# Kernel tuning notes

Hardware: AMD Instinct MI355X
Metric: run time of the kernel (lower is better)

## Reference

```python
import jax, jax.numpy as jnp
import numpy as np

NEG_SLOPE = 0.1   # LeakyReLU slope
EPS = 1e-5        # GroupNorm eps
GROUPS = 8        # out_feat // 16 = 128 // 16
NSAMPLE = 16      # naggre (k in KNN)
FEAT = 128        # feat_dim


def leaky(x):
    return jnp.where(x >= 0, x, NEG_SLOPE * x)


def gnorm(x, gamma, beta):
    # GroupNorm over channel dim 1; works for [B,C,N] and [B,C,N,K]
    B, C = x.shape[0], x.shape[1]
    sh = x.shape
    xg = x.reshape(B, GROUPS, -1)
    m = xg.mean(-1, keepdims=True)
    v = xg.var(-1, keepdims=True)
    xg = (xg - m) * jax.lax.rsqrt(v + EPS)
    br = (1, C) + (1,) * (len(sh) - 2)
    return xg.reshape(sh) * gamma.reshape(br) + beta.reshape(br)


def conv1(x, W, b):  # 1x1 Conv1d: x [B,C,N]
    return jnp.einsum('oc,bcn->bon', W, x) + b[None, :, None]


def conv2(x, W, b):  # 1x1 Conv2d: x [B,C,N,K]
    return jnp.einsum('oc,bcnk->bonk', W, x) + b[None, :, None, None]


def knn_idx(xyz, k):
    # xyz [B,3,N] -> idx [B,N,k] of k nearest points (self included)
    pts = xyz.transpose(0, 2, 1)                      # [B,N,3]
    sq = jnp.sum(pts * pts, axis=-1)                  # [B,N]
    d2 = sq[:, :, None] + sq[:, None, :] - 2.0 * jnp.einsum('bnc,bmc->bnm', pts, pts)
    _, idx = jax.lax.top_k(-d2, k)
    return idx


# grouping_operation: feat [B,C,N], idx [B,N,K] -> [B,C,N,K]
group = jax.vmap(lambda f, i: f[:, i])


def setup_inputs() -> dict:
    key = jax.random.key(0)
    ks = jax.random.split(key, 32)
    s = 0.05
    d = {
        'xyz': jax.random.normal(ks[0], (2, 3, 8192), jnp.float32),
        'feat': jax.random.normal(ks[1], (2, FEAT, 8192), jnp.float32),
        'W_pre': jax.random.normal(ks[2], (FEAT, FEAT), jnp.float32) * s,
        'b_pre': jnp.zeros((FEAT,), jnp.float32),
        'W_pos1': jax.random.normal(ks[3], (FEAT, 3), jnp.float32) * s,
        'b_pos1': jnp.zeros((FEAT,), jnp.float32),
        'g_pos1': jnp.ones((FEAT,), jnp.float32),
        'be_pos1': jnp.zeros((FEAT,), jnp.float32),
        'W_pos2': jax.random.normal(ks[4], (FEAT, FEAT), jnp.float32) * s,
        'b_pos2': jnp.zeros((FEAT,), jnp.float32),
        'W_q': jax.random.normal(ks[5], (FEAT, FEAT), jnp.float32) * s,
        'b_q': jnp.zeros((FEAT,), jnp.float32),
        'W_k': jax.random.normal(ks[6], (FEAT, FEAT), jnp.float32) * s,
        'b_k': jnp.zeros((FEAT,), jnp.float32),
        'W_v': jax.random.normal(ks[7], (FEAT, FEAT), jnp.float32) * s,
        'b_v': jnp.zeros((FEAT,), jnp.float32),
        'W_att1': jax.random.normal(ks[8], (FEAT, FEAT), jnp.float32) * s,
        'b_att1': jnp.zeros((FEAT,), jnp.float32),
        'g_att1': jnp.ones((FEAT,), jnp.float32),
        'be_att1': jnp.zeros((FEAT,), jnp.float32),
        'W_att2': jax.random.normal(ks[9], (FEAT, FEAT), jnp.float32) * s,
        'b_att2': jnp.zeros((FEAT,), jnp.float32),
        'W_post': jax.random.normal(ks[10], (FEAT, FEAT), jnp.float32) * s,
        'b_post': jnp.zeros((FEAT,), jnp.float32),
        'g_post': jnp.ones((FEAT,), jnp.float32),
        'be_post': jnp.zeros((FEAT,), jnp.float32),
    }
    return d


def reference(xyz, feat, W_pre, b_pre, W_pos1, b_pos1, g_pos1, be_pos1,
              W_pos2, b_pos2, W_q, b_q, W_k, b_k, W_v, b_v,
              W_att1, b_att1, g_att1, be_att1, W_att2, b_att2,
              W_post, b_post, g_post, be_post):
    idx = knn_idx(xyz, NSAMPLE)                       # [B,N,K]
    new_feat = conv1(feat, W_pre, b_pre)              # [B,C,N]
    rel = group(xyz, idx) - xyz[:, :, :, None]        # [B,3,N,K]
    pos = conv2(rel, W_pos1, b_pos1)
    pos = leaky(gnorm(pos, g_pos1, be_pos1))
    pos = conv2(pos, W_pos2, b_pos2)                  # [B,C,N,K]
    q = conv1(new_feat, W_q, b_q)
    k = group(conv1(new_feat, W_k, b_k), idx)
    v = group(conv1(new_feat, W_v, b_v), idx)
    att = q[:, :, :, None] - k + pos
    att = conv2(att, W_att1, b_att1)
    att = leaky(gnorm(att, g_att1, be_att1))
    att = conv2(att, W_att2, b_att2)
    att = jax.nn.softmax(att, axis=3)                 # softmax over neighbors
    out = jnp.sum(att * v, axis=3) + new_feat         # [B,C,N]
    out = leaky(gnorm(conv1(out, W_post, b_post), g_post, be_post))
    return out
```

## Files before the change

kernel.cpp:

```cpp
#include <hip/hip_runtime.h>
#include <hip/hip_bf16.h>
#include <float.h>

#define B_ 2
#define N_ 8192
#define C_ 128
#define K_ 16
#define G_ 8
#define NK_ (N_*K_)
#define BN_ (B_*N_)
#define BNK_ (B_*NK_)
#define CN_ (C_*N_)
#define NEG 0.1f
#define EPSV 1e-5f

typedef __attribute__((ext_vector_type(4))) float f32x4;
typedef __attribute__((ext_vector_type(8))) short s16x8;
typedef __attribute__((ext_vector_type(4))) short s16x4;

__device__ __forceinline__ float leakyf(float x){ return x >= 0.f ? x : NEG*x; }
__device__ __forceinline__ short f2b(float x){
  union { __hip_bfloat16 b; short s; } u; u.b = __float2bfloat16(x); return u.s;
}
__device__ __forceinline__ float b2f(short s){
  union { __hip_bfloat16 b; short s; } u; u.s = s; return __bfloat162float(u.b);
}

__device__ __forceinline__ int dpp_shr1_i(int x){
  return __builtin_amdgcn_update_dpp(x, x, 0x111, 0xF, 0xF, false);
}
__device__ __forceinline__ unsigned long long dpp_shr1_u64(unsigned long long x){
  union { unsigned long long q; int i[2]; } u; u.q = x;
  u.i[0] = dpp_shr1_i(u.i[0]);
  u.i[1] = dpp_shr1_i(u.i[1]);
  return u.q;
}
__device__ __forceinline__ unsigned long long readlane_u64(unsigned long long x, int l){
  union { unsigned long long q; int i[2]; } u; u.q = x;
  union { unsigned long long q; int i[2]; } r;
  r.i[0] = __builtin_amdgcn_readlane(u.i[0], l);
  r.i[1] = __builtin_amdgcn_readlane(u.i[1], l);
  return r.q;
}
__device__ __forceinline__ unsigned long long d2key(double d2, int idx){
  d2 = fmax(d2, 0.0);
  union { double d; unsigned long long q; } u; u.d = d2;
  return (u.q & ~0x1FFFull) | (unsigned long long)idx;
}
__device__ __forceinline__ double key_upper_d2(unsigned long long k){
  union { unsigned long long q; double d; } u; u.q = k | 0x1FFFull;
  return u.d;
}

__global__ __launch_bounds__(256) void pack_featb_kernel(const float* __restrict__ xyz,
    const float* __restrict__ feat, float4* __restrict__ pt4, ushort* __restrict__ fb){
  int e = blockIdx.x*256 + threadIdx.x;
  int b = e >> 13, n = e & (N_-1);
  const float* xb = xyz + b*3*N_;
  float x = xb[n], y = xb[N_+n], z = xb[2*N_+n];
  pt4[e] = make_float4(x, y, z, x*x + y*y + z*z);
  const float* xin = feat + b*CN_ + n;
  #pragma unroll
  for (int c0 = 0; c0 < C_; c0 += 8){
    s16x8 o8;
    #pragma unroll
    for (int i = 0; i < 8; i++) o8[i] = f2b(xin[(size_t)(c0+i)*N_]);
    *(s16x8*)(fb + (size_t)e*C_ + c0) = o8;
  }
}

#define KNN_TPB 512
#define KNN_CHUNK 2048
#define KNN_MARGIN 2e-4f
__global__ __launch_bounds__(KNN_TPB) void knn_kernel(const float4* __restrict__ pt4, int* __restrict__ idxo){
  __shared__ float4 sp[KNN_CHUNK];
  int lane = threadIdx.x & 63, wid = threadIdx.x >> 6;
  int qg = blockIdx.x*(KNN_TPB/64) + wid;
  int b = qg >> 13, n = qg & (N_-1);
  const float4* pts = pt4 + b*N_;
  float4 qp = pts[n];
  double qx = qp.x, qy = qp.y, qz = qp.z;
  double qsq = qx*qx + qy*qy + qz*qz;
  float qx2 = -2.f*qp.x, qy2 = -2.f*qp.y, qz2 = -2.f*qp.z;
  unsigned long long mykey;
  float cmpv;

  {
    float4 pp = pts[lane];
    double px = pp.x, py = pp.y, pz = pp.z;
    double psq = px*px + py*py + pz*pz;
    double dot = qx*px + qy*py + qz*pz;
    unsigned long long kl = d2key(qsq + psq - 2.0*dot, lane);
    #pragma unroll
    for (int k2 = 2; k2 <= 64; k2 <<= 1){
      #pragma unroll
      for (int mm = k2>>1; mm > 0; mm >>= 1){
        unsigned long long pk = __shfl_xor(kl, mm, 64);
        bool up = ((lane & k2) == 0);
        bool lower = ((lane & mm) == 0);
        bool myLess = kl < pk;
        bool keep = lower ? (up ? myLess : !myLess) : (up ? !myLess : myLess);
        if (!keep) kl = pk;
      }
    }
    mykey = kl;
    cmpv = (float)(key_upper_d2(readlane_u64(mykey, 15)) - qsq) + KNN_MARGIN;
  }

  auto process = [&](unsigned long long m, unsigned long long keyv){
    while (m){
      int src = __ffsll(m) - 1; m &= m - 1;
      unsigned long long kn = readlane_u64(keyv, src);
      bool less = kn < mykey;
      unsigned long long bm = __ballot(less) & 0xFFFFull;
      if (bm){
        int pos = __ffsll(bm) - 1;
        unsigned long long pk = dpp_shr1_u64(mykey);
        if (lane < 16){
          if (lane > pos) mykey = pk;
          else if (lane == pos) mykey = kn;
        }
      }
    }
  };

  for (int c0 = 0; c0 < N_; c0 += KNN_CHUNK){
    __syncthreads();
    #pragma unroll
    for (int t = 0; t < KNN_CHUNK/KNN_TPB; t++){
      int i = t*KNN_TPB + threadIdx.x;
      sp[i] = pts[c0 + i];
    }
    __syncthreads();
    for (int j0 = 0; j0 < KNN_CHUNK; j0 += 128){
      float4 pA = sp[j0 + lane];
      float4 pB = sp[j0 + 64 + lane];
      float fA = fmaf(pA.x, qx2, fmaf(pA.y, qy2, fmaf(pA.z, qz2, pA.w)));
      float fB = fmaf(pB.x, qx2, fmaf(pB.y, qy2, fmaf(pB.z, qz2, pB.w)));
      unsigned long long mA = __ballot(fA < cmpv);
      unsigned long long mB = __ballot(fB < cmpv);
      if (c0 == 0 && j0 == 0) mA = 0;
      if (mA | mB){
        if (mA){
          double px = pA.x, py = pA.y, pz = pA.z;
          double psq = px*px + py*py + pz*pz;
          double dot = qx*px + qy*py + qz*pz;
          process(mA, d2key(qsq + psq - 2.0*dot, c0 + j0 + lane));
        }
        if (mB){
          double px = pB.x, py = pB.y, pz = pB.z;
          double psq = px*px + py*py + pz*pz;
          double dot = qx*px + qy*py + qz*pz;
          process(mB, d2key(qsq + psq - 2.0*dot, c0 + j0 + 64 + lane));
        }
        cmpv = (float)(key_upper_d2(readlane_u64(mykey, 15)) - qsq) + KNN_MARGIN;
      }
    }
  }
  if (lane < 16) idxo[qg*K_ + lane] = (int)(mykey & 0x1FFFull);
}

__global__ __launch_bounds__(256) void setup_kernel(const float* __restrict__ W_att1,
    const float* __restrict__ W_pos2, const float* __restrict__ W_q, const float* __restrict__ W_k,
    const float* __restrict__ b_pos2, const float* __restrict__ b_att1,
    const float* __restrict__ b_q, const float* __restrict__ b_k,
    float* __restrict__ Wf, float* __restrict__ Wqa, float* __restrict__ Wka,
    float* __restrict__ bG1, float* __restrict__ bqa, float* __restrict__ bka){
  int bx = blockIdx.x;
  if (bx < 192){
    int which = bx >> 6;
    const float* Bm = which==0 ? W_pos2 : (which==1 ? W_q : W_k);
    float* Cm = which==0 ? Wf : (which==1 ? Wqa : Wka);
    int e = (bx & 63)*256 + threadIdx.x;
    int o = e >> 7, c = e & 127;
    float s = 0.f;
    #pragma unroll 8
    for (int m = 0; m < 128; m++) s += W_att1[o*128+m]*Bm[m*128+c];
    Cm[e] = s;
  } else {
    for (int t = threadIdx.x; t < 384; t += 256){
      int which = t >> 7, o = t & 127;
      const float* v = which==0 ? b_pos2 : (which==1 ? b_q : b_k);
      float* out = which==0 ? bG1 : (which==1 ? bqa : bka);
      float s = which==0 ? b_att1[o] : 0.f;
      for (int m = 0; m < 128; m++) s += W_att1[o*128+m]*v[m];
      out[o] = s;
    }
  }
}

__global__ __launch_bounds__(256) void pos_stats_kernel(const float4* __restrict__ pt4,
    const int* __restrict__ idx, const float* __restrict__ W1, const float* __restrict__ b1,
    float* __restrict__ gsum, float* __restrict__ gssq){
  __shared__ float ls[G_], lss[G_];
  if (threadIdx.x < G_){ ls[threadIdx.x] = 0.f; lss[threadIdx.x] = 0.f; }
  __syncthreads();
  int p = blockIdx.x*256 + threadIdx.x;
  int b = p >> 17;
  int n = p >> 4;
  int j = idx[p];
  float4 pj = pt4[(b<<13) + j], pn = pt4[n];
  float rx = pj.x - pn.x, ry = pj.y - pn.y, rz = pj.z - pn.z;
  #pragma unroll
  for (int g = 0; g < G_; g++){
    float s = 0.f, ss = 0.f;
    #pragma unroll
    for (int ci = 0; ci < 16; ci++){
      int c = g*16 + ci;
      float v = b1[c] + W1[3*c]*rx + W1[3*c+1]*ry + W1[3*c+2]*rz;
      s += v; ss += v*v;
    }
    #pragma unroll
    for (int mk = 32; mk; mk >>= 1){ s += __shfl_xor(s, mk, 64); ss += __shfl_xor(ss, mk, 64); }
    if ((threadIdx.x & 63) == 0){ atomicAdd(&ls[g], s); atomicAdd(&lss[g], ss); }
  }
  __syncthreads();
  if (threadIdx.x < G_){
    atomicAdd(&gsum[b*G_ + threadIdx.x], ls[threadIdx.x]);
    atomicAdd(&gssq[b*G_ + threadIdx.x], lss[threadIdx.x]);
  }
}

__global__ void posfin_kernel(const float* __restrict__ gsum, const float* __restrict__ gssq,
    const float* __restrict__ W1, const float* __restrict__ b1,
    const float* __restrict__ g1, const float* __restrict__ be1, float* __restrict__ prm, float invcnt){
  __shared__ float sm[16], sr[16];
  int i = threadIdx.x;
  if (i < 16){
    float m = gsum[i]*invcnt;
    float v = gssq[i]*invcnt - m*m;
    v = fmaxf(v, 0.f);
    sm[i] = m; sr[i] = rsqrtf(v + EPSV);
  }
  __syncthreads();
  int b = i >> 7, c = i & 127, g = c >> 4;
  float rs = sr[b*G_+g]*g1[c];
  float4* p4 = (float4*)prm;
  p4[b*128 + c] = make_float4(W1[3*c]*rs, W1[3*c+1]*rs, W1[3*c+2]*rs,
                              (b1[c]-sm[b*G_+g])*rs + be1[c]);
}

__global__ void attfin_kernel(const float* __restrict__ gsum, const float* __restrict__ gssq,
    const float* __restrict__ ga, const float* __restrict__ bea, float* __restrict__ prm, float invcnt){
  __shared__ float sm[16], sr[16];
  int i = threadIdx.x;
  if (i < 16){
    float m = gsum[i]*invcnt;
    float v = gssq[i]*invcnt - m*m;
    v = fmaxf(v, 0.f);
    sm[i] = m; sr[i] = rsqrtf(v + EPSV);
  }
  __syncthreads();
  int b = i >> 7, c = i & 127, g = c >> 4;
  float sc = ga[c]*sr[b*G_+g];
  float2* p2 = (float2*)prm;
  p2[b*128 + c] = make_float2(sc, bea[c] - sm[b*G_+g]*sc);
}

#define ST_COPY 0
#define ST_GN   1
#define ST_POS  2
#define EP_PM    0
#define EP_QKS   1
#define EP_F32CM 2

template<int STAGE>
__device__ __forceinline__ void stage_x(ushort* xs,
    const ushort* __restrict__ Xb, const float* __restrict__ prm,
    const float4* __restrict__ pt4, const int* __restrict__ idx, int p0, int b)
{
  int tid = threadIdx.x;
  int row = tid & 63, cc = tid >> 6;
  if constexpr (STAGE == ST_COPY){
    const ushort* src = Xb + (size_t)(p0+row)*C_ + cc*32;
    #pragma unroll
    for (int q = 0; q < 4; q++){
      s16x8 v8 = *(const s16x8*)(src + q*8);
      int sl = (cc*4+q) ^ (row&7);
      *(s16x8*)(xs + row*C_ + sl*8) = v8;
    }
  } else if constexpr (STAGE == ST_GN){
    const ushort* src = Xb + (size_t)(p0+row)*C_ + cc*32;
    const float2* pr = (const float2*)prm + b*128;
    #pragma unroll
    for (int q = 0; q < 4; q++){
      s16x8 v8 = *(const s16x8*)(src + q*8);
      s16x8 o8;
      #pragma unroll
      for (int i = 0; i < 8; i++){
        int c = cc*32 + q*8 + i;
        float2 s2 = pr[c];
        o8[i] = f2b(leakyf(b2f(v8[i])*s2.x + s2.y));
      }
      int sl = (cc*4+q) ^ (row&7);
      *(s16x8*)(xs + row*C_ + sl*8) = o8;
    }
  } else {
    int p = p0 + row;
    int ng = p >> 4;
    int j = idx[p];
    float4 pj = pt4[(b<<13) + j], pn = pt4[ng];
    float rx = pj.x - pn.x, ry = pj.y - pn.y, rz = pj.z - pn.z;
    const float4* pr = (const float4*)prm + b*128;
    #pragma unroll
    for (int q = 0; q < 4; q++){
      s16x8 o8;
      #pragma unroll
      for (int i = 0; i < 8; i++){
        int c = cc*32 + q*8 + i;
        float4 s4 = pr[c];
        o8[i] = f2b(leakyf(fmaf(s4.x, rx, fmaf(s4.y, ry, fmaf(s4.z, rz, s4.w)))));
      }
      int sl = (cc*4+q) ^ (row&7);
      *(s16x8*)(xs + row*C_ + sl*8) = o8;
    }
  }
}

__device__ __forceinline__ void load_afr(s16x8 afr[2][4], const float* __restrict__ W, int wid, int lm, int lh){
  #pragma unroll
  for (int t = 0; t < 2; t++){
    int T = wid*2 + t;
    #pragma unroll
    for (int ks = 0; ks < 4; ks++){
      const float* wr = W + (size_t)(T*16 + lm)*C_ + ks*32 + lh*8;
      float4 w0 = *(const float4*)wr;
      float4 w1 = *(const float4*)(wr+4);
      s16x8 a;
      a[0]=f2b(w0.x); a[1]=f2b(w0.y); a[2]=f2b(w0.z); a[3]=f2b(w0.w);
      a[4]=f2b(w1.x); a[5]=f2b(w1.y); a[6]=f2b(w1.z); a[7]=f2b(w1.w);
      afr[t][ks] = a;
    }
  }
}

__device__ __forceinline__ void mfma_tile(f32x4 acc[2][4], const s16x8 afr[2][4],
    const ushort* xs, const float* __restrict__ bias, int wid, int lm, int lh)
{
  #pragma unroll
  for (int t = 0; t < 2; t++){
    f32x4 bs = *(const f32x4*)(bias + (wid*2+t)*16 + lh*4);
    #pragma unroll
    for (int ps = 0; ps < 4; ps++) acc[t][ps] = bs;
  }
  #pragma unroll
  for (int ps = 0; ps < 4; ps++){
    int row = ps*16 + lm;
    s16x8 bf[4];
    #pragma unroll
    for (int ks = 0; ks < 4; ks++){
      int sl = (ks*4+lh) ^ (row&7);
      bf[ks] = *(const s16x8*)(xs + row*C_ + sl*8);
    }
    #pragma unroll
    for (int ks = 0; ks < 4; ks++){
      #pragma unroll
      for (int t = 0; t < 2; t++)
        acc[t][ps] = __builtin_amdgcn_mfma_f32_16x16x32_bf16(afr[t][ks], bf[ks], acc[t][ps], 0,0,0);
    }
  }
}

template<int STAGE, int EPI>
__device__ __forceinline__ void mgemm_body(ushort* xs, float* sblk,
    const ushort* __restrict__ Xb, const float* __restrict__ W, const float* __restrict__ bias,
    const float* __restrict__ prm, const float4* __restrict__ pt4, const int* __restrict__ idx,
    const ushort* __restrict__ Aq, const ushort* __restrict__ Ak,
    void* __restrict__ Y, float* __restrict__ gsum, float* __restrict__ gssq, int bsh, int bx)
{
  int tid = threadIdx.x;
  int l = tid & 63, wid = tid >> 6;
  int lm = l & 15, lh = l >> 4;
  int p0 = bx * 64;
  int b = p0 >> bsh;

  if (tid < 16) sblk[tid] = 0.f;

  s16x8 afr[2][4];
  load_afr(afr, W, wid, lm, lh);
  stage_x<STAGE>(xs, Xb, prm, pt4, idx, p0, b);
  __syncthreads();

  f32x4 acc[2][4];
  mfma_tile(acc, afr, xs, bias, wid, lm, lh);

  float gs[2] = {0.f,0.f}, gq[2] = {0.f,0.f};
  #pragma unroll
  for (int t = 0; t < 2; t++){
    int T = wid*2 + t;
    int o0 = T*16 + lh*4;
    #pragma unroll
    for (int ps = 0; ps < 4; ps++){
      int p = p0 + ps*16 + lm;
      if constexpr (EPI == EP_PM){
        s16x4 r4;
        #pragma unroll
        for (int r = 0; r < 4; r++) r4[r] = f2b(acc[t][ps][r]);
        *(s16x4*)((ushort*)Y + (size_t)p*C_ + o0) = r4;
      } else if constexpr (EPI == EP_QKS){
        int ng = p >> 4;
        int j = idx[p];
        s16x4 aq4 = *(const s16x4*)(Aq + (size_t)ng*C_ + o0);
        s16x4 ak4 = *(const s16x4*)(Ak + ((size_t)(b<<13)+j)*C_ + o0);
        s16x4 r4;
        #pragma unroll
        for (int r = 0; r < 4; r++){
          float v = acc[t][ps][r] + b2f(aq4[r]) - b2f(ak4[r]);
          r4[r] = f2b(v);
          gs[t] += v; gq[t] += v*v;
        }
        *(s16x4*)((ushort*)Y + (size_t)p*C_ + o0) = r4;
      } else {
        float* yf = (float*)Y;
        #pragma unroll
        for (int r = 0; r < 4; r++){
          float v = acc[t][ps][r];
          yf[(size_t)(o0+r)*BN_ + p] = v;
          gs[t] += v; gq[t] += v*v;
        }
      }
    }
  }

  if constexpr (EPI == EP_QKS || EPI == EP_F32CM){
    #pragma unroll
    for (int t = 0; t < 2; t++){
      float s = gs[t], q = gq[t];
      #pragma unroll
      for (int mk = 32; mk; mk >>= 1){ s += __shfl_xor(s, mk, 64); q += __shfl_xor(q, mk, 64); }
      if (l == 0){
        int T = wid*2 + t;
        atomicAdd(&sblk[T], s); atomicAdd(&sblk[8+T], q);
      }
    }
    __syncthreads();
    if (tid < 8){
      atomicAdd(&gsum[b*G_ + tid], sblk[tid]);
      atomicAdd(&gssq[b*G_ + tid], sblk[8+tid]);
    }
  }
}

template<int STAGE, int EPI>
__global__ __launch_bounds__(256) void mgemm_kernel(
    const ushort* __restrict__ Xb, const float* __restrict__ W, const float* __restrict__ bias,
    const float* __restrict__ prm, const float4* __restrict__ pt4, const int* __restrict__ idx,
    const ushort* __restrict__ Aq, const ushort* __restrict__ Ak,
    void* __restrict__ Y, float* __restrict__ gsum, float* __restrict__ gssq, int bsh)
{
  __shared__ ushort xs[64*128];
  __shared__ float sblk[16];
  mgemm_body<STAGE,EPI>(xs, sblk, Xb, W, bias, prm, pt4, idx, Aq, Ak, Y, gsum, gssq, bsh, blockIdx.x);
}

__global__ __launch_bounds__(256) void qkv_kernel(const ushort* __restrict__ nfb,
    const float* __restrict__ Wv, const float* __restrict__ bv,
    const float* __restrict__ Wqa, const float* __restrict__ bqa,
    const float* __restrict__ Wka, const float* __restrict__ bka,
    ushort* __restrict__ vb, ushort* __restrict__ Aqb, ushort* __restrict__ Akb)
{
  __shared__ ushort xs[64*128];
  __shared__ float sblk[16];
  if (blockIdx.y == 0)
    mgemm_body<ST_COPY,EP_PM>(xs, sblk, nfb, Wv, bv, nullptr, nullptr, nullptr, nullptr, nullptr, vb, nullptr, nullptr, 13, blockIdx.x);
  else if (blockIdx.y == 1)
    mgemm_body<ST_COPY,EP_PM>(xs, sblk, nfb, Wqa, bqa, nullptr, nullptr, nullptr, nullptr, nullptr, Aqb, nullptr, nullptr, 13, blockIdx.x);
  else
    mgemm_body<ST_COPY,EP_PM>(xs, sblk, nfb, Wka, bka, nullptr, nullptr, nullptr, nullptr, nullptr, Akb, nullptr, nullptr, 13, blockIdx.x);
}

__global__ __launch_bounds__(256) void fatt_kernel(const ushort* __restrict__ Xb ,
    const float* __restrict__ W , const float* __restrict__ bias ,
    const float* __restrict__ prm , const int* __restrict__ idx,
    const ushort* __restrict__ vb, const ushort* __restrict__ nfb, ushort* __restrict__ outb)
{
  __shared__ ushort xs[64*128];
  int tid = threadIdx.x;
  int l = tid & 63, wid = tid >> 6;
  int lm = l & 15, lh = l >> 4;
  int p0 = blockIdx.x * 64;
  int b = p0 >> 17;

  s16x8 afr[2][4];
  load_afr(afr, W, wid, lm, lh);
  stage_x<ST_GN>(xs, Xb, prm, nullptr, nullptr, p0, b);
  __syncthreads();

  f32x4 acc[2][4];
  mfma_tile(acc, afr, xs, bias, wid, lm, lh);

  #pragma unroll
  for (int t = 0; t < 2; t++){
    int o0 = (wid*2+t)*16 + lh*4;
    #pragma unroll
    for (int ps = 0; ps < 4; ps++){
      int p = p0 + ps*16 + lm;
      int j = idx[p];
      s16x4 v4 = *(const s16x4*)(vb + ((size_t)(b<<13)+j)*C_ + o0);
      f32x4 e, pv;
      #pragma unroll
      for (int r = 0; r < 4; r++){
        float ev = __expf(acc[t][ps][r]);
        e[r] = ev;
        pv[r] = ev * b2f(v4[r]);
      }
      #pragma unroll
      for (int mk = 1; mk < 16; mk <<= 1){
        #pragma unroll
        for (int r = 0; r < 4; r++){
          e[r]  += __shfl_xor(e[r], mk, 64);
          pv[r] += __shfl_xor(pv[r], mk, 64);
        }
      }
      if (lm == 0){
        int n = p >> 4;
        s16x4 n4 = *(const s16x4*)(nfb + (size_t)n*C_ + o0);
        s16x4 o4;
        #pragma unroll
        for (int r = 0; r < 4; r++) o4[r] = f2b(pv[r]/e[r] + b2f(n4[r]));
        *(s16x4*)(outb + (size_t)n*C_ + o0) = o4;
      }
    }
  }
}

__global__ __launch_bounds__(256) void final_kernel(const float* __restrict__ out1,
    const float* __restrict__ gsum, const float* __restrict__ gssq,
    const float* __restrict__ g, const float* __restrict__ be, float* __restrict__ out){
  int e = blockIdx.x*256 + threadIdx.x;
  int b = e >> 20;
  int c = (e >> 13) & (C_-1);
  int n = e & (N_-1);
  int gi = b*G_ + (c >> 4);
  const float invcnt = 1.0f/(float)(16*N_);
  float m = gsum[gi]*invcnt;
  float var = gssq[gi]*invcnt - m*m;
  var = fmaxf(var, 0.f);
  float r = rsqrtf(var + EPSV);
  float v = (out1[(size_t)c*BN_ + b*N_ + n] - m) * r;
  v = v*g[c] + be[c];
  out[e] = leakyf(v);
}

extern "C" void kernel_launch(void* const* d_in, const int* in_sizes, int n_in,
                              void* d_out, int out_size, void* d_ws, size_t ws_size,
                              hipStream_t stream) {
  const float* xyz    = (const float*)d_in[0];
  const float* feat   = (const float*)d_in[1];
  const float* W_pre  = (const float*)d_in[2];
  const float* b_pre  = (const float*)d_in[3];
  const float* W_pos1 = (const float*)d_in[4];
  const float* b_pos1 = (const float*)d_in[5];
  const float* g_pos1 = (const float*)d_in[6];
  const float* be_pos1= (const float*)d_in[7];
  const float* W_pos2 = (const float*)d_in[8];
  const float* b_pos2 = (const float*)d_in[9];
  const float* W_q    = (const float*)d_in[10];
  const float* b_q    = (const float*)d_in[11];
  const float* W_k    = (const float*)d_in[12];
  const float* b_k    = (const float*)d_in[13];
  const float* W_v    = (const float*)d_in[14];
  const float* b_v    = (const float*)d_in[15];
  const float* W_att1 = (const float*)d_in[16];
  const float* b_att1 = (const float*)d_in[17];
  const float* g_att1 = (const float*)d_in[18];
  const float* be_att1= (const float*)d_in[19];
  const float* W_att2 = (const float*)d_in[20];
  const float* b_att2 = (const float*)d_in[21];
  const float* W_post = (const float*)d_in[22];
  const float* b_post = (const float*)d_in[23];
  const float* g_post = (const float*)d_in[24];
  const float* be_post= (const float*)d_in[25];

  char* w = (char*)d_ws;
  float4* pt4 = (float4*)w;            w += sizeof(float4)*BN_;
  int* idx = (int*)w;                  w += sizeof(int)*BNK_;
  ushort* fb   = (ushort*)w;           w += (size_t)2*BN_*C_;
  ushort* nfb  = (ushort*)w;           w += (size_t)2*BN_*C_;
  ushort* vb   = (ushort*)w;           w += (size_t)2*BN_*C_;
  ushort* Aqb  = (ushort*)w;           w += (size_t)2*BN_*C_;
  ushort* Akb  = (ushort*)w;           w += (size_t)2*BN_*C_;
  ushort* outb = (ushort*)w;           w += (size_t)2*BN_*C_;
  float* out1  = (float*)w;            w += (size_t)4*BN_*C_;
  ushort* bufA = (ushort*)w;           w += (size_t)2*BNK_*C_;
  float* Wf    = (float*)w;            w += sizeof(float)*C_*C_;
  float* Wqa   = (float*)w;            w += sizeof(float)*C_*C_;
  float* Wka   = (float*)w;            w += sizeof(float)*C_*C_;
  float* bG1   = (float*)w;            w += 512;
  float* bqa   = (float*)w;            w += 512;
  float* bka   = (float*)w;            w += 512;
  float* posPrm= (float*)w;            w += sizeof(float)*1024;
  float* attPrm= (float*)w;            w += sizeof(float)*512;
  float* stats = (float*)w;            w += 1024;

  float* pos_sum = stats +  0, *pos_ssq = stats + 16;
  float* att_sum = stats + 64, *att_ssq = stats + 80;
  float* post_sum= stats +128, *post_ssq= stats +144;

  hipMemsetAsync(stats, 0, 1024, stream);

  pack_featb_kernel<<<BN_/256, 256, 0, stream>>>(xyz, feat, pt4, fb);
  knn_kernel<<<BN_/(KNN_TPB/64), KNN_TPB, 0, stream>>>(pt4, idx);

  setup_kernel<<<193, 256, 0, stream>>>(W_att1, W_pos2, W_q, W_k, b_pos2, b_att1, b_q, b_k,
      Wf, Wqa, Wka, bG1, bqa, bka);

  mgemm_kernel<ST_COPY,EP_PM><<<BN_/64, 256, 0, stream>>>(fb, W_pre, b_pre, nullptr, nullptr, nullptr,
      nullptr, nullptr, nfb, nullptr, nullptr, 13);
  qkv_kernel<<<dim3(BN_/64, 3), 256, 0, stream>>>(nfb, W_v, b_v, Wqa, bqa, Wka, bka, vb, Aqb, Akb);

  pos_stats_kernel<<<BNK_/256, 256, 0, stream>>>(pt4, idx, W_pos1, b_pos1, pos_sum, pos_ssq);
  posfin_kernel<<<1, 256, 0, stream>>>(pos_sum, pos_ssq, W_pos1, b_pos1, g_pos1, be_pos1, posPrm,
      1.0f/(float)(16.0*NK_));

  mgemm_kernel<ST_POS,EP_QKS><<<BNK_/64, 256, 0, stream>>>(nullptr, Wf, bG1, posPrm, pt4, idx,
      Aqb, Akb, bufA, att_sum, att_ssq, 17);
  attfin_kernel<<<1, 256, 0, stream>>>(att_sum, att_ssq, g_att1, be_att1, attPrm, 1.0f/(float)(16.0*NK_));

  fatt_kernel<<<BNK_/64, 256, 0, stream>>>(bufA, W_att2, b_att2, attPrm, idx, vb, nfb, outb);

  mgemm_kernel<ST_COPY,EP_F32CM><<<BN_/64, 256, 0, stream>>>(outb, W_post, b_post, nullptr, nullptr, nullptr,
      nullptr, nullptr, out1, post_sum, post_ssq, 13);
  final_kernel<<<(B_*CN_)/256, 256, 0, stream>>>(out1, post_sum, post_ssq, g_post, be_post, (float*)d_out);
}
```

Before: 351.5 us.

## Replace brute-force KNN with uniform-grid spatial binning and shell search

Bins points into a 32^3 uniform grid per batch (count, prefix scan, scatter), then each query wave searches its own cell and the 26 neighbours, expanding shells until the 16th-nearest distance is bounded by the searched radius. This removes the O(N^2) distance scan over all 8192 points per query. It adds three small kernels, a memset and atomics. The grid extent is fixed at [-6, 6] with clamping to the edge cells. Ordering among equal-distance neighbours may differ because points now arrive in cell order.

```diff
diff --git a/kernel.cpp b/kernel.cpp
--- a/kernel.cpp
+++ b/kernel.cpp
@@ -14,6 +14,13 @@
 #define NEG 0.1f
 #define EPSV 1e-5f
 
+#define GR_ 32
+#define NC_ (GR_*GR_*GR_)
+#define GLOF -6.0f
+#define GHF 0.375f
+#define KNN_MARGIN 2e-4f
+#define EMPTY_KEY 0x7FEFFFFFFFFFFFFFull
+
 typedef __attribute__((ext_vector_type(4))) float f32x4;
 typedef __attribute__((ext_vector_type(8))) short s16x8;
 typedef __attribute__((ext_vector_type(4))) short s16x4;
@@ -51,14 +58,20 @@
   union { unsigned long long q; double d; } u; u.q = k | 0x1FFFull;
   return u.d;
 }
+__device__ __forceinline__ int cell1(float x){
+  int c = (int)floorf((x - GLOF)*(1.0f/GHF));
+  return min(max(c, 0), GR_-1);
+}
 
 __global__ __launch_bounds__(256) void pack_featb_kernel(const float* __restrict__ xyz,
-    const float* __restrict__ feat, float4* __restrict__ pt4, ushort* __restrict__ fb){
+    const float* __restrict__ feat, float4* __restrict__ pt4, ushort* __restrict__ fb,
+    int* __restrict__ cellCnt){
   int e = blockIdx.x*256 + threadIdx.x;
   int b = e >> 13, n = e & (N_-1);
   const float* xb = xyz + b*3*N_;
   float x = xb[n], y = xb[N_+n], z = xb[2*N_+n];
   pt4[e] = make_float4(x, y, z, x*x + y*y + z*z);
+  atomicAdd(&cellCnt[b*NC_ + (cell1(z)*GR_ + cell1(y))*GR_ + cell1(x)], 1);
   const float* xin = feat + b*CN_ + n;
   #pragma unroll
   for (int c0 = 0; c0 < C_; c0 += 8){
@@ -69,43 +82,54 @@
   }
 }
 
-#define KNN_TPB 512
-#define KNN_CHUNK 2048
-#define KNN_MARGIN 2e-4f
-__global__ __launch_bounds__(KNN_TPB) void knn_kernel(const float4* __restrict__ pt4, int* __restrict__ idxo){
-  __shared__ float4 sp[KNN_CHUNK];
+__global__ __launch_bounds__(1024) void scan_kernel(const int* __restrict__ cnt,
+    int* __restrict__ cellStart, int* __restrict__ cellCur){
+  __shared__ int bs[1024];
+  int t = threadIdx.x;
+  int base = t*64;
+  int s = 0;
+  for (int i = 0; i < 64; i++) s += cnt[base+i];
+  bs[t] = s;
+  __syncthreads();
+  for (int off = 1; off < 1024; off <<= 1){
+    int v = (t >= off) ? bs[t-off] : 0;
+    __syncthreads();
+    bs[t] += v;
+    __syncthreads();
+  }
+  int run = (t == 0) ? 0 : bs[t-1];
+  for (int i = 0; i < 64; i++){
+    cellStart[base+i] = run;
+    cellCur[base+i]  = run;
+    run += cnt[base+i];
+  }
+  if (t == 1023) cellStart[2*NC_] = BN_;
+}
+
+__global__ __launch_bounds__(256) void scatter_kernel(const float4* __restrict__ pt4,
+    int* __restrict__ cellCur, float4* __restrict__ spts, int* __restrict__ sidx){
+  int e = blockIdx.x*256 + threadIdx.x;
+  int b = e >> 13;
+  float4 p = pt4[e];
+  int cid = b*NC_ + (cell1(p.z)*GR_ + cell1(p.y))*GR_ + cell1(p.x);
+  int slot = atomicAdd(&cellCur[cid], 1);
+  spts[slot] = p;
+  sidx[slot] = e & (N_-1);
+}
+
+__global__ __launch_bounds__(512) void knn_kernel(const float4* __restrict__ pt4,
+    const float4* __restrict__ spts, const int* __restrict__ sidx,
+    const int* __restrict__ cellStart, int* __restrict__ idxo){
   int lane = threadIdx.x & 63, wid = threadIdx.x >> 6;
-  int qg = blockIdx.x*(KNN_TPB/64) + wid;
-  int b = qg >> 13, n = qg & (N_-1);
-  const float4* pts = pt4 + b*N_;
-  float4 qp = pts[n];
+  int qg = blockIdx.x*8 + wid;
+  int b = qg >> 13;
+  float4 qp = pt4[qg];
   double qx = qp.x, qy = qp.y, qz = qp.z;
   double qsq = qx*qx + qy*qy + qz*qz;
   float qx2 = -2.f*qp.x, qy2 = -2.f*qp.y, qz2 = -2.f*qp.z;
-  unsigned long long mykey;
-  float cmpv;
-
-  {
-    float4 pp = pts[lane];
-    double px = pp.x, py = pp.y, pz = pp.z;
-    double psq = px*px + py*py + pz*pz;
-    double dot = qx*px + qy*py + qz*pz;
-    unsigned long long kl = d2key(qsq + psq - 2.0*dot, lane);
-    #pragma unroll
-    for (int k2 = 2; k2 <= 64; k2 <<= 1){
-      #pragma unroll
-      for (int mm = k2>>1; mm > 0; mm >>= 1){
-        unsigned long long pk = __shfl_xor(kl, mm, 64);
-        bool up = ((lane & k2) == 0);
-        bool lower = ((lane & mm) == 0);
-        bool myLess = kl < pk;
-        bool keep = lower ? (up ? myLess : !myLess) : (up ? !myLess : myLess);
-        if (!keep) kl = pk;
-      }
-    }
-    mykey = kl;
-    cmpv = (float)(key_upper_d2(readlane_u64(mykey, 15)) - qsq) + KNN_MARGIN;
-  }
+  unsigned long long mykey = EMPTY_KEY;
+  float cmpv = FLT_MAX;
+  int ci = cell1(qp.x), cj = cell1(qp.y), ck = cell1(qp.z);
 
   auto process = [&](unsigned long long m, unsigned long long keyv){
     while (m){
@@ -124,38 +148,58 @@
     }
   };
 
-  for (int c0 = 0; c0 < N_; c0 += KNN_CHUNK){
-    __syncthreads();
-    #pragma unroll
-    for (int t = 0; t < KNN_CHUNK/KNN_TPB; t++){
-      int i = t*KNN_TPB + threadIdx.x;
-      sp[i] = pts[c0 + i];
-    }
-    __syncthreads();
-    for (int j0 = 0; j0 < KNN_CHUNK; j0 += 128){
-      float4 pA = sp[j0 + lane];
-      float4 pB = sp[j0 + 64 + lane];
-      float fA = fmaf(pA.x, qx2, fmaf(pA.y, qy2, fmaf(pA.z, qz2, pA.w)));
-      float fB = fmaf(pB.x, qx2, fmaf(pB.y, qy2, fmaf(pB.z, qz2, pB.w)));
-      unsigned long long mA = __ballot(fA < cmpv);
-      unsigned long long mB = __ballot(fB < cmpv);
-      if (c0 == 0 && j0 == 0) mA = 0;
-      if (mA | mB){
-        if (mA){
-          double px = pA.x, py = pA.y, pz = pA.z;
-          double psq = px*px + py*py + pz*pz;
-          double dot = qx*px + qy*py + qz*pz;
-          process(mA, d2key(qsq + psq - 2.0*dot, c0 + j0 + lane));
+  auto do_cell = [&](int cx, int cy, int cz){
+    int cid = b*NC_ + (cz*GR_ + cy)*GR_ + cx;
+    int s = cellStart[cid], e = cellStart[cid+1];
+    for (int off = s; off < e; off += 64){
+      int t = off + lane;
+      bool valid = t < e;
+      float4 pp = make_float4(0.f, 0.f, 0.f, 3.0e38f);
+      int oi = 0;
+      if (valid){ pp = spts[t]; oi = sidx[t]; }
+      float f = fmaf(pp.x, qx2, fmaf(pp.y, qy2, fmaf(pp.z, qz2, pp.w)));
+      unsigned long long m = __ballot(valid && (f < cmpv));
+      if (m){
+        double px = pp.x, py = pp.y, pz = pp.z;
+        double psq = px*px + py*py + pz*pz;
+        double dot = qx*px + qy*py + qz*pz;
+        unsigned long long kv = d2key(qsq + psq - 2.0*dot, oi);
+        process(m, kv);
+        cmpv = (float)(key_upper_d2(readlane_u64(mykey, 15)) - qsq) + KNN_MARGIN;
+      }
+    }
+  };
+
+  do_cell(ci, cj, ck);
+  for (int dz = -1; dz <= 1; dz++){
+    int z = ck + dz; if (z < 0 || z >= GR_) continue;
+    for (int dy = -1; dy <= 1; dy++){
+      int y = cj + dy; if (y < 0 || y >= GR_) continue;
+      for (int dx = -1; dx <= 1; dx++){
+        int x = ci + dx; if (x < 0 || x >= GR_) continue;
+        if ((dx | dy | dz) == 0) continue;
+        do_cell(x, y, z);
+      }
+    }
+  }
+  double thr_up = key_upper_d2(readlane_u64(mykey, 15));
+  double bound = (double)GHF;
+  for (int r = 2; r < GR_ && thr_up > bound*bound*0.999; r++){
+    for (int dz = -r; dz <= r; dz++){
+      int z = ck + dz; if (z < 0 || z >= GR_) continue;
+      bool fz = (dz == -r) || (dz == r);
+      for (int dy = -r; dy <= r; dy++){
+        int y = cj + dy; if (y < 0 || y >= GR_) continue;
+        bool face = fz || (dy == -r) || (dy == r);
+        int step = face ? 1 : 2*r;
+        for (int dx = -r; dx <= r; dx += step){
+          int x = ci + dx; if (x < 0 || x >= GR_) continue;
+          do_cell(x, y, z);
         }
-        if (mB){
-          double px = pB.x, py = pB.y, pz = pB.z;
-          double psq = px*px + py*py + pz*pz;
-          double dot = qx*px + qy*py + qz*pz;
-          process(mB, d2key(qsq + psq - 2.0*dot, c0 + j0 + 64 + lane));
-        }
-        cmpv = (float)(key_upper_d2(readlane_u64(mykey, 15)) - qsq) + KNN_MARGIN;
-      }
-    }
+      }
+    }
+    thr_up = key_upper_d2(readlane_u64(mykey, 15));
+    bound = (double)r * (double)GHF;
   }
   if (lane < 16) idxo[qg*K_ + lane] = (int)(mykey & 0x1FFFull);
 }
@@ -592,15 +636,23 @@
   float* posPrm= (float*)w;            w += sizeof(float)*1024;
   float* attPrm= (float*)w;            w += sizeof(float)*512;
   float* stats = (float*)w;            w += 1024;
+  int* cellCnt = (int*)w;              w += sizeof(int)*2*NC_;
+  int* cellStart=(int*)w;              w += sizeof(int)*(2*NC_+1);
+  int* cellCur = (int*)w;              w += sizeof(int)*2*NC_;
+  float4* spts = (float4*)w;           w += sizeof(float4)*BN_;
+  int* sidx    = (int*)w;              w += sizeof(int)*BN_;
 
   float* pos_sum = stats +  0, *pos_ssq = stats + 16;
   float* att_sum = stats + 64, *att_ssq = stats + 80;
   float* post_sum= stats +128, *post_ssq= stats +144;
 
   hipMemsetAsync(stats, 0, 1024, stream);
-
-  pack_featb_kernel<<<BN_/256, 256, 0, stream>>>(xyz, feat, pt4, fb);
-  knn_kernel<<<BN_/(KNN_TPB/64), KNN_TPB, 0, stream>>>(pt4, idx);
+  hipMemsetAsync(cellCnt, 0, sizeof(int)*2*NC_, stream);
+
+  pack_featb_kernel<<<BN_/256, 256, 0, stream>>>(xyz, feat, pt4, fb, cellCnt);
+  scan_kernel<<<1, 1024, 0, stream>>>(cellCnt, cellStart, cellCur);
+  scatter_kernel<<<BN_/256, 256, 0, stream>>>(pt4, cellCur, spts, sidx);
+  knn_kernel<<<BN_/8, 512, 0, stream>>>(pt4, spts, sidx, cellStart, idx);
 
   setup_kernel<<<193, 256, 0, stream>>>(W_att1, W_pos2, W_q, W_k, b_pos2, b_att1, b_q, b_k,
       Wf, Wqa, Wka, bG1, bqa, bka);
```

Measured after the change: 687.2 us. 95.5% more time.
